# Performance work log

Hardware: AMD Instinct MI355X
Metric: run time of the kernel (lower is better)

Reference implementation:

```python
import jax, jax.numpy as jnp
import numpy as np
import math

B, C_GT, H, W = 32, 1, 256, 1216
SH, SW = 16, 48  # samplesH, samplesW (eval-mode jitter fixed at 0)


def _gauss_kernel():
    # kernel_size = [int(2H/(SH+1)), int(2W/(SW+1))], sigma = size/3 (per original code)
    kh = int(2 * H / (SH + 1))
    kw = int(2 * W / (SW + 1))
    sh = 2 * H / (SH + 1) / 3.0
    sw = 2 * W / (SW + 1) / 3.0
    gh = np.exp(-(((np.arange(kh) - (kh - 1) / 2) / sh) ** 2) / 2) / (sh * math.sqrt(2 * math.pi))
    gw = np.exp(-(((np.arange(kw) - (kw - 1) / 2) / sw) ** 2) / 2) / (sw * math.sqrt(2 * math.pi))
    k = np.outer(gh, gw)
    k = k / k.sum()
    return jnp.asarray(k, jnp.float32)


def _grid_sample_bilinear(img, grid):
    # img [B,C,H,W]; grid [B,Hs,Ws,2] with (x,y) in [-1,1].
    # Matches F.grid_sample(mode='bilinear', padding_mode='zeros', align_corners=False).
    Bb, C, Hh, Ww = img.shape
    x = (grid[..., 0] + 1.0) * Ww / 2.0 - 0.5
    y = (grid[..., 1] + 1.0) * Hh / 2.0 - 0.5
    x0 = jnp.floor(x); y0 = jnp.floor(y)
    x1 = x0 + 1.0;     y1 = y0 + 1.0
    wx1 = x - x0; wx0 = 1.0 - wx1
    wy1 = y - y0; wy0 = 1.0 - wy1
    imt = img.transpose(0, 2, 3, 1)  # [B,H,W,C]
    bidx = jnp.arange(Bb)[:, None, None]

    def gather(yc, xc, wgt):
        m = (yc >= 0) & (yc <= Hh - 1) & (xc >= 0) & (xc <= Ww - 1)
        yi = jnp.clip(yc, 0, Hh - 1).astype(jnp.int32)
        xi = jnp.clip(xc, 0, Ww - 1).astype(jnp.int32)
        v = imt[bidx, yi, xi]  # [B,Hs,Ws,C]
        return v * (wgt * m)[..., None]

    out = (gather(y0, x0, wy0 * wx0) + gather(y0, x1, wy0 * wx1)
           + gather(y1, x0, wy1 * wx0) + gather(y1, x1, wy1 * wx1))
    return out.transpose(0, 3, 1, 2)  # [B,C,Hs,Ws]


def _forward(gt, dense_vector_field):
    # GaussianSmooth: grouped VALID conv with a big separable Gaussian kernel
    k = _gauss_kernel()
    kern = jnp.broadcast_to(k[None, None], (2, 1, k.shape[0], k.shape[1]))
    smoothed = jax.lax.conv_general_dilated(dense_vector_field, kern, (1, 1), 'VALID',
                                            feature_group_count=2)  # [B,2,H',W']
    # F.interpolate(mode='nearest') to (SH, SW): idx = floor(i * in / out)
    hi = np.arange(SH) * smoothed.shape[2] // SH
    wi = np.arange(SW) * smoothed.shape[3] // SW
    svf = smoothed[:, :, hi][:, :, :, wi]  # [B,2,SH,SW]

    # WarpSample base grid (x first, then y — grid_sample convention)
    gw, gh = np.meshgrid(np.linspace(-(SW - 1) / SW, (SW - 1) / SW, SW),
                         np.linspace(-(SH - 1) / SH, (SH - 1) / SH, SH))
    norm_grid = jnp.asarray(np.stack((gw, gh), 2), jnp.float32)  # [SH,SW,2]
    grid_to_sample = svf.transpose(0, 2, 3, 1) + norm_grid  # [B,SH,SW,2]

    gt_sampled = _grid_sample_bilinear(gt, grid_to_sample)  # [B,1,SH,SW]

    # expand(): vectorized scatter replacing the per-pixel Python loop.
    row = jnp.clip(((grid_to_sample[..., 1] + 1.0) / 2.0 * H).astype(jnp.int32), 0, H - 1)
    col = jnp.clip(((grid_to_sample[..., 0] + 1.0) / 2.0 * W).astype(jnp.int32), 0, W - 1)
    bidx = jnp.arange(gt.shape[0])[:, None, None]
    sparse = jnp.zeros((gt.shape[0], H, W, gt.shape[1]), gt.dtype)
    sparse = sparse.at[bidx, row, col].set(gt_sampled.transpose(0, 2, 3, 1))
    sparse = sparse.transpose(0, 3, 1, 2)  # [B,1,H,W]
    # eval-mode KITTI: zero the top 96 rows (no LiDAR returns there)
    sparse = sparse.at[:, :, 0:96, :].set(0.0)
    return sparse, dense_vector_field.transpose(0, 2, 3, 1), grid_to_sample


def setup_inputs():
    key = jax.random.key(0)
    k1, k2 = jax.random.split(key)
    gt = jax.random.uniform(k1, (B, C_GT, H, W), dtype=jnp.float32) * 80.0  # KITTI depth range
    dense_vector_field = jax.random.normal(k2, (B, 2, H, W), dtype=jnp.float32) * 0.1
    return {"gt": gt, "dense_vector_field": dense_vector_field}


def reference(gt, dense_vector_field):
    return _forward(gt, dense_vector_field)
```

## Files before the change

### kernel.cpp

```cpp
#include <hip/hip_runtime.h>
#include <math.h>

#ifndef M_PI
#define M_PI 3.14159265358979323846
#endif

#define Hh   256
#define Ww   1216
#define HWsz (Hh * Ww)
#define Bb   32
#define KH   30
#define KW   49
#define NTAP (KH * KW)
#define SHs  16
#define SWs  48
#define NPB  (SHs * SWs)
#define NPTS (Bb * NPB)
#define OUT0 (Bb * HWsz)
#define OUT1 (Bb * HWsz * 2)

#define CONV_BLKS (NPTS / 4)
#define TPOS_BLKS (Bb * (HWsz / 4) / 256)

__device__ __forceinline__ float samp4(const float* __restrict__ g, float yc, float xc, float w) {
#pragma clang fp contract(off)
    bool m = (yc >= 0.0f) && (yc <= 255.0f) && (xc >= 0.0f) && (xc <= 1215.0f);
    float ycl = fminf(fmaxf(yc, 0.0f), 255.0f);
    float xcl = fminf(fmaxf(xc, 0.0f), 1215.0f);
    int yi = (int)ycl, xi = (int)xcl;
    float wm = m ? w : 0.0f;
    return g[yi * Ww + xi] * wm;
}

__global__ __launch_bounds__(256) void k_fused(
    const float* __restrict__ gt, const float* __restrict__ dvf,
    float* __restrict__ out0, float* __restrict__ out1, float* __restrict__ out2,
    float* __restrict__ vbuf, int* __restrict__ rcbuf)
{
#pragma clang fp contract(off)
    const int tid = threadIdx.x;

    if (blockIdx.x >= CONV_BLKS) {
        const size_t idx = (size_t)(blockIdx.x - CONV_BLKS) * 256 + tid;
        ((float4*)out0)[idx] = make_float4(0.0f, 0.0f, 0.0f, 0.0f);
        const int b = (int)(idx / (HWsz / 4));
        const int r = (int)(idx - (size_t)b * (HWsz / 4));
        const float4* p0 = (const float4*)(dvf + (size_t)b * 2 * HWsz);
        const float4* p1 = (const float4*)(dvf + (size_t)b * 2 * HWsz + HWsz);
        float4 a = p0[r], c = p1[r];
        float4* o = (float4*)(out1 + ((size_t)b * HWsz + (size_t)r * 4) * 2);
        o[0] = make_float4(a.x, c.x, a.y, c.y);
        o[1] = make_float4(a.z, c.z, a.w, c.w);
        return;
    }

    __shared__ double s_gh[KH];
    __shared__ double s_gw[KW];
    __shared__ double s_invS;
    __shared__ float  s_w[NTAP];
    __shared__ int    s_off[NTAP];

    if (tid < KH) {
        const double sh_ = (2.0 * 256.0 / 17.0) / 3.0;
        double u = ((double)tid - 14.5) / sh_;
        s_gh[tid] = exp(-(u * u) / 2.0) / (sh_ * sqrt(2.0 * M_PI));
    } else if (tid >= 64 && tid < 64 + KW) {
        int t = tid - 64;
        const double sw_ = (2.0 * 1216.0 / 49.0) / 3.0;
        double u = ((double)t - 24.0) / sw_;
        s_gw[t] = exp(-(u * u) / 2.0) / (sw_ * sqrt(2.0 * M_PI));
    }
    __syncthreads();
    if (tid == 0) {
        double a = 0.0, c = 0.0;
        for (int t = 0; t < KH; ++t) a += s_gh[t];
        for (int t = 0; t < KW; ++t) c += s_gw[t];
        s_invS = 1.0 / (a * c);
    }
    __syncthreads();
    {
        const double invS = s_invS;
        for (int t = tid; t < NTAP; t += 256) {
            int dy = t / KW, dx = t - dy * KW;
            s_w[t]   = (float)((s_gh[dy] * s_gw[dx]) * invS);
            s_off[t] = dy * Ww + dx;
        }
    }
    __syncthreads();

    const int wave = tid >> 6, lane = tid & 63;
    const int pt = blockIdx.x * 4 + wave;
    const int b = pt / NPB, p = pt - b * NPB;
    const int i = p / SWs, j = p - i * SWs;
    const int y0r = (i * 227) >> 4;
    const int x0c = (j * 1168) / 48;
    const float* c0 = dvf + (size_t)b * (2 * HWsz) + y0r * Ww + x0c;
    const float* c1 = c0 + HWsz;

    double a0 = 0.0, a1 = 0.0;
    for (int t = lane; t < NTAP; t += 64) {
        int off = s_off[t];
        double w = (double)s_w[t];
        a0 += w * (double)c0[off];
        a1 += w * (double)c1[off];
    }
    for (int o = 32; o > 0; o >>= 1) {
        a0 += __shfl_down(a0, o);
        a1 += __shfl_down(a1, o);
    }

    if (lane == 0) {
        float sx = (float)a0, sy = (float)a1;
        const double startw = -(47.0 / 48.0), stopw = 47.0 / 48.0;
        const double starth = -(15.0 / 16.0), stoph = 15.0 / 16.0;
        const double stepw = (stopw - startw) / 47.0;
        const double steph = (stoph - starth) / 15.0;
        float gwl = (j == SWs - 1) ? (float)stopw : (float)((double)j * stepw + startw);
        float ghl = (i == SHs - 1) ? (float)stoph : (float)((double)i * steph + starth);
        float gx = sx + gwl;
        float gy = sy + ghl;

        float* o2 = out2 + ((size_t)(b * SHs + i) * SWs + j) * 2;
        o2[0] = gx; o2[1] = gy;

        const float* gtb = gt + (size_t)b * HWsz;
        float xw = (gx + 1.0f) * 1216.0f; xw = xw / 2.0f; xw = xw - 0.5f;
        float yw = (gy + 1.0f) * 256.0f;  yw = yw / 2.0f; yw = yw - 0.5f;
        float x0f = floorf(xw), y0f = floorf(yw);
        float x1f = x0f + 1.0f, y1f = y0f + 1.0f;
        float wx1 = xw - x0f, wx0 = 1.0f - wx1;
        float wy1 = yw - y0f, wy0 = 1.0f - wy1;
        float v = samp4(gtb, y0f, x0f, wy0 * wx0) + samp4(gtb, y0f, x1f, wy0 * wx1)
                + samp4(gtb, y1f, x0f, wy1 * wx0) + samp4(gtb, y1f, x1f, wy1 * wx1);

        float rf = (gy + 1.0f) / 2.0f * 256.0f;
        float cf = (gx + 1.0f) / 2.0f * 1216.0f;
        int row = (int)rf; row = row < 0 ? 0 : (row > Hh - 1 ? Hh - 1 : row);
        int col = (int)cf; col = col < 0 ? 0 : (col > Ww - 1 ? Ww - 1 : col);
        vbuf[pt]  = v;
        rcbuf[pt] = (row << 16) | col;
    }
}

__global__ __launch_bounds__(256) void k_scatter(
    const float* __restrict__ vbuf, const int* __restrict__ rcbuf, float* __restrict__ out0)
{
    __shared__ float sv[NPB];
    __shared__ int   sr[NPB];
    const int b = blockIdx.x, tid = threadIdx.x;
    for (int t = tid; t < NPB; t += 256) {
        sv[t] = vbuf[b * NPB + t];
        sr[t] = rcbuf[b * NPB + t];
    }
    __syncthreads();
    float* o = out0 + (size_t)b * HWsz;
    for (int p = tid; p < NPB; p += 256) {
        int rc = sr[p];
        int r = rc >> 16;
        if (r < 96) continue;
        bool win = true;
        for (int q = p + 1; q < NPB; ++q) {
            if (sr[q] == rc) { win = false; break; }
        }
        if (win) o[r * Ww + (rc & 0xffff)] = sv[p];
    }
}

extern "C" void kernel_launch(void* const* d_in, const int* in_sizes, int n_in,
                              void* d_out, int out_size, void* d_ws, size_t ws_size,
                              hipStream_t stream) {
    const float* gt  = (const float*)d_in[0];
    const float* dvf = (const float*)d_in[1];
    float* out0 = (float*)d_out;
    float* out1 = out0 + OUT0;
    float* out2 = out1 + OUT1;
    float* vbuf  = (float*)d_ws;
    int*   rcbuf = (int*)d_ws + NPTS;

    hipLaunchKernelGGL(k_fused, dim3(CONV_BLKS + TPOS_BLKS), dim3(256), 0, stream,
                       gt, dvf, out0, out1, out2, vbuf, rcbuf);
    hipLaunchKernelGGL(k_scatter, dim3(Bb), dim3(256), 0, stream,
                       vbuf, rcbuf, out0);
}
```

Measured before the change: 293.5 us.

## Precompute Gaussian weight table in a separate kernel and vectorize conv taps

Moves the per-block Gaussian weight and offset table construction into a one-block pre-kernel that writes the weights to workspace, so each conv block no longer does double-precision exp and several barriers. The tap loop now processes four consecutive columns per lane with 16-byte vector loads of weights and input, with a separate tail pass for the last kernel column. This adds a kernel launch and relies on memcpy-based unaligned vector loads, since the row offsets and the 49-wide weight rows are not 16-byte aligned.

```diff
diff --git a/kernel.cpp b/kernel.cpp
--- a/kernel.cpp
+++ b/kernel.cpp
@@ -22,6 +22,8 @@
 #define CONV_BLKS (NPTS / 4)
 #define TPOS_BLKS (Bb * (HWsz / 4) / 256)
 
+typedef float f4 __attribute__((ext_vector_type(4)));
+
 __device__ __forceinline__ float samp4(const float* __restrict__ g, float yc, float xc, float w) {
 #pragma clang fp contract(off)
     bool m = (yc >= 0.0f) && (yc <= 255.0f) && (xc >= 0.0f) && (xc <= 1215.0f);
@@ -32,33 +34,11 @@
     return g[yi * Ww + xi] * wm;
 }
 
-__global__ __launch_bounds__(256) void k_fused(
-    const float* __restrict__ gt, const float* __restrict__ dvf,
-    float* __restrict__ out0, float* __restrict__ out1, float* __restrict__ out2,
-    float* __restrict__ vbuf, int* __restrict__ rcbuf)
-{
-#pragma clang fp contract(off)
-    const int tid = threadIdx.x;
-
-    if (blockIdx.x >= CONV_BLKS) {
-        const size_t idx = (size_t)(blockIdx.x - CONV_BLKS) * 256 + tid;
-        ((float4*)out0)[idx] = make_float4(0.0f, 0.0f, 0.0f, 0.0f);
-        const int b = (int)(idx / (HWsz / 4));
-        const int r = (int)(idx - (size_t)b * (HWsz / 4));
-        const float4* p0 = (const float4*)(dvf + (size_t)b * 2 * HWsz);
-        const float4* p1 = (const float4*)(dvf + (size_t)b * 2 * HWsz + HWsz);
-        float4 a = p0[r], c = p1[r];
-        float4* o = (float4*)(out1 + ((size_t)b * HWsz + (size_t)r * 4) * 2);
-        o[0] = make_float4(a.x, c.x, a.y, c.y);
-        o[1] = make_float4(a.z, c.z, a.w, c.w);
-        return;
-    }
-
+__global__ __launch_bounds__(256) void k_weights(float* __restrict__ wtab) {
     __shared__ double s_gh[KH];
     __shared__ double s_gw[KW];
     __shared__ double s_invS;
-    __shared__ float  s_w[NTAP];
-    __shared__ int    s_off[NTAP];
+    const int tid = threadIdx.x;
 
     if (tid < KH) {
         const double sh_ = (2.0 * 256.0 / 17.0) / 3.0;
@@ -78,15 +58,33 @@
         s_invS = 1.0 / (a * c);
     }
     __syncthreads();
-    {
-        const double invS = s_invS;
-        for (int t = tid; t < NTAP; t += 256) {
-            int dy = t / KW, dx = t - dy * KW;
-            s_w[t]   = (float)((s_gh[dy] * s_gw[dx]) * invS);
-            s_off[t] = dy * Ww + dx;
-        }
-    }
-    __syncthreads();
+    const double invS = s_invS;
+    for (int t = tid; t < NTAP; t += 256)
+        wtab[t] = (float)((s_gh[t / KW] * s_gw[t % KW]) * invS);
+}
+
+__global__ __launch_bounds__(256) void k_fused(
+    const float* __restrict__ gt, const float* __restrict__ dvf,
+    const float* __restrict__ wtab,
+    float* __restrict__ out0, float* __restrict__ out1, float* __restrict__ out2,
+    float* __restrict__ vbuf, int* __restrict__ rcbuf)
+{
+#pragma clang fp contract(off)
+    const int tid = threadIdx.x;
+
+    if (blockIdx.x >= CONV_BLKS) {
+        const size_t idx = (size_t)(blockIdx.x - CONV_BLKS) * 256 + tid;
+        ((float4*)out0)[idx] = make_float4(0.0f, 0.0f, 0.0f, 0.0f);
+        const int b = (int)(idx / (HWsz / 4));
+        const int rr = (int)(idx - (size_t)b * (HWsz / 4));
+        const float4* p0 = (const float4*)(dvf + (size_t)b * 2 * HWsz);
+        const float4* p1 = (const float4*)(dvf + (size_t)b * 2 * HWsz + HWsz);
+        float4 a = p0[rr], c = p1[rr];
+        float4* o = (float4*)(out1 + ((size_t)b * HWsz + (size_t)rr * 4) * 2);
+        o[0] = make_float4(a.x, c.x, a.y, c.y);
+        o[1] = make_float4(a.z, c.z, a.w, c.w);
+        return;
+    }
 
     const int wave = tid >> 6, lane = tid & 63;
     const int pt = blockIdx.x * 4 + wave;
@@ -98,9 +96,26 @@
     const float* c1 = c0 + HWsz;
 
     double a0 = 0.0, a1 = 0.0;
-    for (int t = lane; t < NTAP; t += 64) {
-        int off = s_off[t];
-        double w = (double)s_w[t];
+#pragma unroll
+    for (int rq = 0; rq < 6; ++rq) {
+        int q = lane + 64 * rq;
+        if (q < 360) {
+            int dy = q / 12, qx = q - dy * 12;
+            int off = dy * Ww + qx * 4;
+            int tq  = dy * KW + qx * 4;
+            f4 wq, va, vb;
+            __builtin_memcpy(&wq, wtab + tq, 16);
+            __builtin_memcpy(&va, c0 + off, 16);
+            __builtin_memcpy(&vb, c1 + off, 16);
+            a0 += (double)wq.x * (double)va.x; a1 += (double)wq.x * (double)vb.x;
+            a0 += (double)wq.y * (double)va.y; a1 += (double)wq.y * (double)vb.y;
+            a0 += (double)wq.z * (double)va.z; a1 += (double)wq.z * (double)vb.z;
+            a0 += (double)wq.w * (double)va.w; a1 += (double)wq.w * (double)vb.w;
+        }
+    }
+    if (lane < KH) {
+        int off = lane * Ww + 48;
+        double w = (double)wtab[lane * KW + 48];
         a0 += w * (double)c0[off];
         a1 += w * (double)c1[off];
     }
@@ -176,9 +191,11 @@
     float* out2 = out1 + OUT1;
     float* vbuf  = (float*)d_ws;
     int*   rcbuf = (int*)d_ws + NPTS;
-
+    float* wtab  = (float*)d_ws + 2 * NPTS;
+
+    hipLaunchKernelGGL(k_weights, dim3(1), dim3(256), 0, stream, wtab);
     hipLaunchKernelGGL(k_fused, dim3(CONV_BLKS + TPOS_BLKS), dim3(256), 0, stream,
-                       gt, dvf, out0, out1, out2, vbuf, rcbuf);
+                       gt, dvf, wtab, out0, out1, out2, vbuf, rcbuf);
     hipLaunchKernelGGL(k_scatter, dim3(Bb), dim3(256), 0, stream,
                        vbuf, rcbuf, out0);
 }
```

Result: no change. 293.3 us (-0.1%).
